# Kernel optimization log

Hardware: AMD Instinct MI355X
Metric: run time of the kernel (lower is better)

The kernel has to match this reference:

```python
import jax, jax.numpy as jnp
import numpy as np

SPARQ = 32
NEG = -32000.0


def sparq_masked_bmm(a, b, xs, xs_mask, value):
    # a: [N,A,B], b: [N,C,B], xs/xs_mask: [N,A,Z]
    N, A, B = a.shape
    C = b.shape[1]
    xs = jnp.clip(xs, 0, C - 1)
    _, a_idx = jax.lax.top_k(jnp.abs(a), SPARQ)              # SparQ: keep top-32 |q| dims
    a_mask = jnp.zeros_like(a).at[
        jnp.arange(N)[:, None, None], jnp.arange(A)[None, :, None], a_idx].set(1.0)
    ts = jnp.einsum('nab,ncb->nac', a * a_mask, b)           # [N,A,C]
    ys = jnp.take_along_axis(ts, xs, axis=-1)                # [N,A,Z]
    return jnp.where(xs_mask > 0.5, ys, value)


def forward_mask(w0, k_budget, q, k):
    # q: [NH, A, HID], k: [NH, T_SRC, HID]; returns additive mask [NH, A, T_SRC]
    NH, A, HID = q.shape
    T_SRC = k.shape[1]
    start = T_SRC - A + 1
    tsrcs_f = jnp.arange(start, start + A).astype(jnp.float32)   # [A]
    ws = jnp.full((A,), float(w0), jnp.float32)
    Zc = 2 * k_budget + 8                                        # static cap on unique pixel count
    z = jnp.arange(Zc)
    pixels = jnp.broadcast_to(jnp.where(z < k_budget, z, 0)[None, None, :], (NH, A, Zc)).astype(jnp.int32)
    pmask = jnp.broadcast_to((z < w0).astype(jnp.float32)[None, None, :], (NH, A, Zc))
    need = (ws < tsrcs_f)[None, :, None]                         # computed ONCE, as in torch
    w = w0
    while True:  # static python loop: w doubles until T_SRC
        txs = jnp.round(pixels * (tsrcs_f / ws)[None, :, None]).astype(jnp.int32)
        scores = sparq_masked_bmm(q, k, txs, pmask, NEG)
        tks = jnp.clip(jnp.round(ws / tsrcs_f * k_budget), 1.0,
                       jnp.minimum(ws - 1.0, float(Zc - 1))).astype(jnp.int32)[None, :, None]
        _, idx = jax.lax.top_k(scores, Zc)
        new_pixels = jnp.take_along_axis(pixels, idx, axis=-1)
        new_mask = (z[None, None, :] < tks).astype(jnp.float32)
        pixels = jnp.where(need, new_pixels, pixels)
        pmask = jnp.where(need, new_mask, pmask)
        # tree doubling: each pixel splits into up to 2 children at the new scale
        ws_new = jnp.minimum(tsrcs_f, ws * 2.0)
        scale = (ws_new / ws)[None, :, None]
        ps_start = jnp.round(pixels * scale).astype(jnp.int32)
        ps_end = jnp.round((pixels + 1) * scale).astype(jnp.int32)
        counts = ps_end - ps_start
        reps = jnp.arange(2, dtype=jnp.float32)[None, None, None, :] * pmask[..., None]
        reps = jnp.minimum(reps, jnp.maximum(counts - 1, 0)[..., None].astype(jnp.float32)).astype(jnp.int32)
        ps = (ps_start[..., None] + reps).reshape(NH * A, Zc * 2)
        # emulate sort + unique_consecutive + compacting scatter (duplicates -> -1 tail)
        ps = jnp.sort(ps, axis=-1)
        is_new = jnp.concatenate([jnp.ones((NH * A, 1), bool), ps[:, 1:] != ps[:, :-1]], axis=1)
        rank = jnp.cumsum(is_new, axis=-1) - 1
        res = jnp.full_like(ps, -1).at[jnp.arange(NH * A)[:, None], rank].set(ps)
        res = res.reshape(NH, A, 2 * Zc)[:, :, :Zc]              # static truncation (valid count <= 2k+1)
        pmask = (res >= 0).astype(jnp.float32)
        pixels = jnp.where(res >= 0, res, 0)
        ws = ws_new
        if w == T_SRC:
            break
        w = min(T_SRC, w * 2)
    pixels = (pixels.astype(jnp.float32) * pmask).astype(jnp.int32)
    ret = jnp.full((NH, A, T_SRC), NEG, jnp.float32)
    ret = ret.at[jnp.arange(NH)[:, None, None], jnp.arange(A)[None, :, None], pixels].set(0.0)
    return ret


def tree_attention(q, k, v, mask, k_budget, w0):
    N, H, T_SRC, HID = k.shape
    T_DST = q.shape[2]
    t_dense = max(0, k_budget - T_SRC + T_DST)
    outs = []
    if t_dense > 0:
        s = jnp.einsum('nhqd,nhkd->nhqk', q[:, :, :t_dense], k) + mask[:, :, :t_dense]
        outs.append(jnp.einsum('nhqk,nhkd->nhqd', jax.nn.softmax(s, axis=-1), v))
    if T_DST - t_dense > 0:
        qs = q[:, :, t_dense:]
        ms = forward_mask(w0, k_budget,
                          qs.reshape(N * H, -1, HID),
                          k.reshape(N * H, T_SRC, HID)).reshape(N, H, -1, T_SRC)
        s = jnp.einsum('nhqd,nhkd->nhqk', qs, k) + mask[:, :, t_dense:] + ms
        outs.append(jnp.einsum('nhqk,nhkd->nhqd', jax.nn.softmax(s, axis=-1), v))
    return jnp.concatenate(outs, axis=2)


def setup_inputs():
    key = jax.random.key(0)
    kq, kk, kv = jax.random.split(key, 3)
    N, H, T, HID = 1, 8, 2048, 64
    q = jax.random.normal(kq, (N, H, T, HID), jnp.float32)
    k = jax.random.normal(kk, (N, H, T, HID), jnp.float32)
    v = jax.random.normal(kv, (N, H, T, HID), jnp.float32)
    causal = jnp.tril(jnp.ones((T, T), bool))
    mask = jnp.where(causal, 0.0, NEG)[None, None].astype(jnp.float32)
    return {"q": q, "k": k, "v": v, "mask": mask}


def reference(q, k, v, mask):
    return tree_attention(q, k, v, mask, 512, 64)
```

## Files before the change

kernel.cpp:

```cpp
#include <hip/hip_runtime.h>
#include <math.h>

constexpr int HID    = 64;
constexpr int TT     = 2048;
constexpr int NHEAD  = 8;
constexpr int TDENSE = 512;
constexpr int ZC     = 1032;
constexpr int BITW   = 1024;

__device__ __forceinline__ float waveSum(float v) {
#pragma unroll
    for (int o = 32; o > 0; o >>= 1) v += __shfl_xor(v, o, 64);
    return v;
}
__device__ __forceinline__ int waveSumI(int v) {
#pragma unroll
    for (int o = 32; o > 0; o >>= 1) v += __shfl_xor(v, o, 64);
    return v;
}
__device__ __forceinline__ float waveMax(float v) {
#pragma unroll
    for (int o = 32; o > 0; o >>= 1) v = fmaxf(v, __shfl_xor(v, o, 64));
    return v;
}
__device__ __forceinline__ unsigned orderKey(float f) {
    unsigned u = __float_as_uint(f);
    return (u & 0x80000000u) ? ~u : (u | 0x80000000u);
}
__device__ __forceinline__ float dot4(float4 a, float4 b) {
    return fmaf(a.x, b.x, fmaf(a.y, b.y, fmaf(a.z, b.z, a.w * b.w)));
}
__device__ __forceinline__ float dotRow64(const float4* __restrict__ kr,
                                          const float4* __restrict__ qs) {
    float s0 = 0.f, s1 = 0.f, s2 = 0.f, s3 = 0.f;
#pragma unroll 2
    for (int i = 0; i < 4; i++) {
        float4 ka = kr[4*i+0], kb = kr[4*i+1], kc = kr[4*i+2], kd = kr[4*i+3];
        float4 qa = qs[4*i+0], qb = qs[4*i+1], qc = qs[4*i+2], qd = qs[4*i+3];
        s0 += dot4(ka, qa); s1 += dot4(kb, qb);
        s2 += dot4(kc, qc); s3 += dot4(kd, qd);
    }
    return (s0 + s1) + (s2 + s3);
}

struct __align__(16) SMem {
    float qf[HID];
    float aq[HID];
    float qm[HID];
    float partial[256];
    unsigned short pixA[ZC];
    unsigned short pixB[ZC];
    unsigned skey[ZC];
    unsigned bitmap[BITW];
    unsigned hist[4][256];
    float red[8];
    int scal[8];
    unsigned wsum[4];
};

__global__ __launch_bounds__(256)
void tree_attn_kernel(const float* __restrict__ q, const float* __restrict__ k,
                      const float* __restrict__ v, float* __restrict__ out) {
    __shared__ SMem sm;
    const int t    = 2047 - (int)blockIdx.x;
    const int h    = blockIdx.y;
    const int tid  = threadIdx.x;
    const int lane = tid & 63;
    const int wave = tid >> 6;
    const int sub  = lane & 15;
    const int grp  = lane >> 4;

    const float* qrow = q + (size_t)(h * TT + t) * HID;
    const float* kh   = k + (size_t)h * TT * HID;
    const float* vh   = v + (size_t)h * TT * HID;
    float*       orow = out + (size_t)(h * TT + t) * HID;

    if (tid < HID) sm.qf[tid] = qrow[tid];
    __syncthreads();

    if (t < TDENSE) {
        const int nk = t + 1;
        float* f = (float*)sm.skey;
        {
            int z = tid;
            for (; z + 256 < nk; z += 512) {
                float s0 = dotRow64((const float4*)(kh + (size_t)z * HID), (const float4*)sm.qf);
                float s1 = dotRow64((const float4*)(kh + (size_t)(z + 256) * HID), (const float4*)sm.qf);
                f[z] = s0; f[z + 256] = s1;
            }
            if (z < nk)
                f[z] = dotRow64((const float4*)(kh + (size_t)z * HID), (const float4*)sm.qf);
        }
        __syncthreads();
        float m = -3.0e38f;
        for (int z = tid; z < nk; z += 256) m = fmaxf(m, f[z]);
        m = waveMax(m);
        if (lane == 0) sm.red[wave] = m;
        __syncthreads();
        m = fmaxf(fmaxf(sm.red[0], sm.red[1]), fmaxf(sm.red[2], sm.red[3]));
        __syncthreads();
        float ls = 0.f;
        for (int z = tid; z < nk; z += 256) { float e = expf(f[z] - m); f[z] = e; ls += e; }
        ls = waveSum(ls);
        if (lane == 0) sm.red[4 + wave] = ls;
        __syncthreads();
        ls = sm.red[4] + sm.red[5] + sm.red[6] + sm.red[7];
        float4 acc = {0.f, 0.f, 0.f, 0.f};
        for (int z = (wave << 2) + grp; z < nk; z += 16) {
            float w = f[z];
            const float4 vv = *reinterpret_cast<const float4*>(vh + (size_t)z * HID + (sub << 2));
            acc.x = fmaf(w, vv.x, acc.x); acc.y = fmaf(w, vv.y, acc.y);
            acc.z = fmaf(w, vv.z, acc.z); acc.w = fmaf(w, vv.w, acc.w);
        }
#pragma unroll
        for (int o = 16; o <= 32; o <<= 1) {
            acc.x += __shfl_xor(acc.x, o, 64); acc.y += __shfl_xor(acc.y, o, 64);
            acc.z += __shfl_xor(acc.z, o, 64); acc.w += __shfl_xor(acc.w, o, 64);
        }
        if (grp == 0) reinterpret_cast<float4*>(sm.partial)[wave * 16 + sub] = acc;
        __syncthreads();
        if (tid < HID) {
            float o = sm.partial[tid] + sm.partial[64 + tid] + sm.partial[128 + tid] + sm.partial[192 + tid];
            orow[tid] = o / ls;
        }
        return;
    }

    const int a     = t - TDENSE;
    const int tsrci = TDENSE + 1 + a;
    const float tsrc = (float)tsrci;

    if (tid < HID) sm.aq[tid] = fabsf(sm.qf[tid]);
    __syncthreads();
    if (tid < HID) {
        float me = sm.aq[tid]; int c = 0;
#pragma unroll
        for (int i = 0; i < HID; i++) {
            float o = sm.aq[i];
            c += (o > me) || (o == me && i < tid);
        }
        sm.qm[tid] = (c < 32) ? sm.qf[tid] : 0.0f;
    }
    for (int z = tid; z < ZC; z += 256) sm.pixA[z] = (z < 512) ? (unsigned short)z : (unsigned short)0;
    for (int z = tid; z < 1024; z += 256) ((unsigned*)sm.hist)[z] = 0;
    __syncthreads();

    unsigned short* cur = sm.pixA;
    unsigned short* nxt = sm.pixB;
    int U = 64;
    float ws = 64.0f;
    int pmaxb = 511;

    for (int it = 0; it < 6; it++) {
        if (ws == tsrc) break;
        const float wsn   = fminf(tsrc, ws * 2.0f);
        const float ratio = tsrc / ws;

        {
            int z = tid;
            for (; z + 256 < U; z += 512) {
                int pA = cur[z], pB = cur[z + 256];
                int txA = min(max((int)rintf((float)pA * ratio), 0), TT - 1);
                int txB = min(max((int)rintf((float)pB * ratio), 0), TT - 1);
                float sA = dotRow64((const float4*)(kh + (size_t)txA * HID), (const float4*)sm.qm);
                float sB = dotRow64((const float4*)(kh + (size_t)txB * HID), (const float4*)sm.qm);
                unsigned kA = orderKey(sA), kB = orderKey(sB);
                sm.skey[z] = kA; sm.skey[z + 256] = kB;
                atomicAdd(&sm.hist[wave][kA >> 24], 1u);
                atomicAdd(&sm.hist[wave][kB >> 24], 1u);
            }
            if (z < U) {
                int p  = cur[z];
                int tx = min(max((int)rintf((float)p * ratio), 0), TT - 1);
                float s = dotRow64((const float4*)(kh + (size_t)tx * HID), (const float4*)sm.qm);
                unsigned kk2 = orderKey(s);
                sm.skey[z] = kk2;
                atomicAdd(&sm.hist[wave][kk2 >> 24], 1u);
            }
        }
        float tkf = rintf((ws / tsrc) * 512.0f);
        tkf = fminf(fmaxf(tkf, 1.0f), fminf(ws - 1.0f, 1031.0f));
        const int tks = (int)tkf;
        __syncthreads();

        unsigned thr = 0u;
        if (tks < U) {
            int bs = 24;
            for (;;) {
                if (wave == 0) {
                    const int i0 = 4 * lane;
                    int c0 = 0, c1 = 0, c2 = 0, c3 = 0;
#pragma unroll
                    for (int w = 0; w < 4; w++) {
                        c0 += (int)sm.hist[w][i0 + 0]; c1 += (int)sm.hist[w][i0 + 1];
                        c2 += (int)sm.hist[w][i0 + 2]; c3 += (int)sm.hist[w][i0 + 3];
                    }
#pragma unroll
                    for (int w = 0; w < 4; w++) {
                        sm.hist[w][i0 + 0] = 0; sm.hist[w][i0 + 1] = 0;
                        sm.hist[w][i0 + 2] = 0; sm.hist[w][i0 + 3] = 0;
                    }
                    const unsigned pref = (bs == 24) ? 0u : (unsigned)sm.scal[1];
                    const int wnt = (bs == 24) ? tks : sm.scal[0];
                    int x = c0 + c1 + c2 + c3;
#pragma unroll
                    for (int o = 1; o < 64; o <<= 1) {
                        int y = __shfl_up(x, o, 64);
                        if (lane >= o) x += y;
                    }
                    const int T = __shfl(x, 63, 64);
                    const int R = T - wnt;
                    int p3 = x, p2 = p3 - c3, p1 = p2 - c2, p0 = p1 - c1, pm1 = p0 - c0;
                    int b = -1, nw = 0, cc = 0;
                    if      (p0 > R && pm1 <= R) { b = i0 + 0; nw = p0 - R; cc = c0; }
                    else if (p1 > R && p0  <= R) { b = i0 + 1; nw = p1 - R; cc = c1; }
                    else if (p2 > R && p1  <= R) { b = i0 + 2; nw = p2 - R; cc = c2; }
                    else if (p3 > R && p2  <= R) { b = i0 + 3; nw = p3 - R; cc = c3; }
                    if (b >= 0) {
                        sm.scal[0] = nw;
                        sm.scal[1] = (int)(pref | ((unsigned)b << bs));
                        sm.scal[2] = cc;
                        sm.scal[3] = (cc == nw || bs == 0) ? 1 : 0;
                    }
                }
                __syncthreads();
                if (sm.scal[3]) { thr = (unsigned)sm.scal[1]; break; }
                const unsigned pref = (unsigned)sm.scal[1];
                bs -= 8;
                for (int z = tid; z < U; z += 256) {
                    unsigned key = sm.skey[z];
                    if ((key >> (bs + 8)) == (pref >> (bs + 8)))
                        atomicAdd(&sm.hist[wave][(key >> bs) & 255u], 1u);
                }
                __syncthreads();
            }
        } else {
            for (int z = tid; z < 1024; z += 256) ((unsigned*)sm.hist)[z] = 0;
        }

        const float scale = wsn / ws;
        const int pmax_new = min(32767, (int)rintf((float)(pmaxb + 1) * scale));
        const int nwords = (pmax_new >> 5) + 1;
        for (int w0 = tid; w0 < nwords; w0 += 256) sm.bitmap[w0] = 0;
        __syncthreads();
        for (int z = tid; z < ZC; z += 256) {
            int p = cur[z];
            float pf = (float)p;
            int ps0 = (int)rintf(pf * scale);
            ps0 = min(ps0, 32767);
            atomicOr(&sm.bitmap[ps0 >> 5], 1u << (ps0 & 31));
            if (z < U && sm.skey[z] >= thr) {
                int ps1 = (int)rintf((pf + 1.0f) * scale);
                if (ps1 - ps0 >= 2) {
                    int ch = min(ps0 + 1, 32767);
                    atomicOr(&sm.bitmap[ch >> 5], 1u << (ch & 31));
                }
            }
        }
        __syncthreads();

        const int base = tid * 4;
        unsigned b0 = (base + 0 < nwords) ? sm.bitmap[base + 0] : 0u;
        unsigned b1 = (base + 1 < nwords) ? sm.bitmap[base + 1] : 0u;
        unsigned b2 = (base + 2 < nwords) ? sm.bitmap[base + 2] : 0u;
        unsigned b3 = (base + 3 < nwords) ? sm.bitmap[base + 3] : 0u;
        int myc = __popc(b0) + __popc(b1) + __popc(b2) + __popc(b3);
        int x = myc;
#pragma unroll
        for (int o = 1; o < 64; o <<= 1) {
            int y = __shfl_up(x, o, 64);
            if (lane >= o) x += y;
        }
        if (lane == 63) sm.wsum[wave] = (unsigned)x;
        __syncthreads();
        int wOff = 0;
        for (int wv = 0; wv < wave; wv++) wOff += (int)sm.wsum[wv];
        const int total = (int)(sm.wsum[0] + sm.wsum[1] + sm.wsum[2] + sm.wsum[3]);
        const int newU = min(total, ZC);
        int pos = wOff + x - myc;
#pragma unroll
        for (int w0 = 0; w0 < 4; w0++) {
            unsigned bits = (w0 == 0) ? b0 : (w0 == 1) ? b1 : (w0 == 2) ? b2 : b3;
            int vbase = (base + w0) << 5;
            while (bits) {
                int b = __ffs(bits) - 1;
                bits &= bits - 1;
                if (pos < ZC) nxt[pos] = (unsigned short)(vbase + b);
                pos++;
            }
        }
        for (int z = newU + tid; z < ZC; z += 256) nxt[z] = 0;
        __syncthreads();

        unsigned short* tmp = cur; cur = nxt; nxt = tmp;
        U = newU;
        ws = wsn;
        pmaxb = pmax_new;
    }

    int ca = 0;
    for (int z = tid; z < U; z += 256) ca += (cur[z] < tsrci) ? 1 : 0;
    ca = waveSumI(ca);
    if (lane == 0) sm.scal[4 + wave] = ca;
    __syncthreads();
    const int Uatt = sm.scal[4] + sm.scal[5] + sm.scal[6] + sm.scal[7];
    __syncthreads();

    float* f = (float*)sm.skey;
    {
        int z = tid;
        for (; z + 256 < Uatt; z += 512) {
            float s0 = dotRow64((const float4*)(kh + (size_t)cur[z] * HID), (const float4*)sm.qf);
            float s1 = dotRow64((const float4*)(kh + (size_t)cur[z + 256] * HID), (const float4*)sm.qf);
            f[z] = s0; f[z + 256] = s1;
        }
        if (z < Uatt)
            f[z] = dotRow64((const float4*)(kh + (size_t)cur[z] * HID), (const float4*)sm.qf);
    }
    __syncthreads();
    float m = -3.0e38f;
    for (int z = tid; z < Uatt; z += 256) m = fmaxf(m, f[z]);
    m = waveMax(m);
    if (lane == 0) sm.red[wave] = m;
    __syncthreads();
    m = fmaxf(fmaxf(sm.red[0], sm.red[1]), fmaxf(sm.red[2], sm.red[3]));
    __syncthreads();
    float ls = 0.f;
    for (int z = tid; z < Uatt; z += 256) { float e = expf(f[z] - m); f[z] = e; ls += e; }
    ls = waveSum(ls);
    if (lane == 0) sm.red[4 + wave] = ls;
    __syncthreads();
    ls = sm.red[4] + sm.red[5] + sm.red[6] + sm.red[7];
    float4 acc = {0.f, 0.f, 0.f, 0.f};
    for (int z = (wave << 2) + grp; z < Uatt; z += 16) {
        float w = f[z];
        const float4 vv = *reinterpret_cast<const float4*>(vh + (size_t)cur[z] * HID + (sub << 2));
        acc.x = fmaf(w, vv.x, acc.x); acc.y = fmaf(w, vv.y, acc.y);
        acc.z = fmaf(w, vv.z, acc.z); acc.w = fmaf(w, vv.w, acc.w);
    }
#pragma unroll
    for (int o = 16; o <= 32; o <<= 1) {
        acc.x += __shfl_xor(acc.x, o, 64); acc.y += __shfl_xor(acc.y, o, 64);
        acc.z += __shfl_xor(acc.z, o, 64); acc.w += __shfl_xor(acc.w, o, 64);
    }
    if (grp == 0) reinterpret_cast<float4*>(sm.partial)[wave * 16 + sub] = acc;
    __syncthreads();
    if (tid < HID) {
        float o = sm.partial[tid] + sm.partial[64 + tid] + sm.partial[128 + tid] + sm.partial[192 + tid];
        orow[tid] = o / ls;
    }
}

extern "C" void kernel_launch(void* const* d_in, const int* in_sizes, int n_in,
                              void* d_out, int out_size, void* d_ws, size_t ws_size,
                              hipStream_t stream) {
    (void)in_sizes; (void)n_in; (void)d_ws; (void)ws_size; (void)out_size;
    const float* q = (const float*)d_in[0];
    const float* k = (const float*)d_in[1];
    const float* v = (const float*)d_in[2];
    float* out = (float*)d_out;
    dim3 grid(TT, NHEAD);
    tree_attn_kernel<<<grid, 256, 0, stream>>>(q, k, v, out);
}
```

Baseline: 1.211 ms.

## Merge bitmap atomics across wave lanes and shrink LDS histogram and bitmap

Result: slower. 1.447 ms (+19.6%).

```diff
diff --git a/kernel.cpp b/kernel.cpp
--- a/kernel.cpp
+++ b/kernel.cpp
@@ -6,7 +6,7 @@
 constexpr int NHEAD  = 8;
 constexpr int TDENSE = 512;
 constexpr int ZC     = 1032;
-constexpr int BITW   = 1024;
+constexpr int BITW   = 520;
 
 __device__ __forceinline__ float waveSum(float v) {
 #pragma unroll
@@ -43,6 +43,19 @@
     return (s0 + s1) + (s2 + s3);
 }
 
+__device__ __forceinline__ void mergedAtomicOr(unsigned* bm, unsigned word, unsigned bits,
+                                               bool valid, int lane) {
+    unsigned w = valid ? word : 0xFFFFFFFFu;
+#pragma unroll
+    for (int off = 1; off < 64; off <<= 1) {
+        unsigned ow = __shfl_down(w, off, 64);
+        unsigned ob = __shfl_down(bits, off, 64);
+        if (ow == w) bits |= ob;
+    }
+    unsigned pw = __shfl_up(w, 1, 64);
+    if (valid && (lane == 0 || pw != w)) atomicOr(&bm[w], bits);
+}
+
 struct __align__(16) SMem {
     float qf[HID];
     float aq[HID];
@@ -52,7 +65,7 @@
     unsigned short pixB[ZC];
     unsigned skey[ZC];
     unsigned bitmap[BITW];
-    unsigned hist[4][256];
+    unsigned hist[256];
     float red[8];
     int scal[8];
     unsigned wsum[4];
@@ -142,7 +155,7 @@
         sm.qm[tid] = (c < 32) ? sm.qf[tid] : 0.0f;
     }
     for (int z = tid; z < ZC; z += 256) sm.pixA[z] = (z < 512) ? (unsigned short)z : (unsigned short)0;
-    for (int z = tid; z < 1024; z += 256) ((unsigned*)sm.hist)[z] = 0;
+    sm.hist[tid] = 0;
     __syncthreads();
 
     unsigned short* cur = sm.pixA;
@@ -166,8 +179,8 @@
                 float sB = dotRow64((const float4*)(kh + (size_t)txB * HID), (const float4*)sm.qm);
                 unsigned kA = orderKey(sA), kB = orderKey(sB);
                 sm.skey[z] = kA; sm.skey[z + 256] = kB;
-                atomicAdd(&sm.hist[wave][kA >> 24], 1u);
-                atomicAdd(&sm.hist[wave][kB >> 24], 1u);
+                atomicAdd(&sm.hist[kA >> 24], 1u);
+                atomicAdd(&sm.hist[kB >> 24], 1u);
             }
             if (z < U) {
                 int p  = cur[z];
@@ -175,7 +188,7 @@
                 float s = dotRow64((const float4*)(kh + (size_t)tx * HID), (const float4*)sm.qm);
                 unsigned kk2 = orderKey(s);
                 sm.skey[z] = kk2;
-                atomicAdd(&sm.hist[wave][kk2 >> 24], 1u);
+                atomicAdd(&sm.hist[kk2 >> 24], 1u);
             }
         }
         float tkf = rintf((ws / tsrc) * 512.0f);
@@ -189,17 +202,10 @@
             for (;;) {
                 if (wave == 0) {
                     const int i0 = 4 * lane;
-                    int c0 = 0, c1 = 0, c2 = 0, c3 = 0;
-#pragma unroll
-                    for (int w = 0; w < 4; w++) {
-                        c0 += (int)sm.hist[w][i0 + 0]; c1 += (int)sm.hist[w][i0 + 1];
-                        c2 += (int)sm.hist[w][i0 + 2]; c3 += (int)sm.hist[w][i0 + 3];
-                    }
-#pragma unroll
-                    for (int w = 0; w < 4; w++) {
-                        sm.hist[w][i0 + 0] = 0; sm.hist[w][i0 + 1] = 0;
-                        sm.hist[w][i0 + 2] = 0; sm.hist[w][i0 + 3] = 0;
-                    }
+                    int c0 = (int)sm.hist[i0 + 0], c1 = (int)sm.hist[i0 + 1];
+                    int c2 = (int)sm.hist[i0 + 2], c3 = (int)sm.hist[i0 + 3];
+                    sm.hist[i0 + 0] = 0; sm.hist[i0 + 1] = 0;
+                    sm.hist[i0 + 2] = 0; sm.hist[i0 + 3] = 0;
                     const unsigned pref = (bs == 24) ? 0u : (unsigned)sm.scal[1];
                     const int wnt = (bs == 24) ? tks : sm.scal[0];
                     int x = c0 + c1 + c2 + c3;
@@ -230,32 +236,36 @@
                 for (int z = tid; z < U; z += 256) {
                     unsigned key = sm.skey[z];
                     if ((key >> (bs + 8)) == (pref >> (bs + 8)))
-                        atomicAdd(&sm.hist[wave][(key >> bs) & 255u], 1u);
+                        atomicAdd(&sm.hist[(key >> bs) & 255u], 1u);
                 }
                 __syncthreads();
             }
         } else {
-            for (int z = tid; z < 1024; z += 256) ((unsigned*)sm.hist)[z] = 0;
+            sm.hist[tid] = 0;
         }
 
         const float scale = wsn / ws;
-        const int pmax_new = min(32767, (int)rintf((float)(pmaxb + 1) * scale));
+        const int pmax_new = min(BITW * 32 - 1, (int)rintf((float)(pmaxb + 1) * scale));
         const int nwords = (pmax_new >> 5) + 1;
         for (int w0 = tid; w0 < nwords; w0 += 256) sm.bitmap[w0] = 0;
         __syncthreads();
-        for (int z = tid; z < ZC; z += 256) {
-            int p = cur[z];
+        for (int z = tid; z < 1280; z += 256) {
+            bool valid = z < ZC;
+            int p = valid ? cur[z] : 0;
+            int ps0 = min((int)rintf((float)p * scale), BITW * 32 - 1);
+            mergedAtomicOr(sm.bitmap, (unsigned)(ps0 >> 5), 1u << (ps0 & 31), valid, lane);
+        }
+        const int Upad = (U + 255) & ~255;
+        for (int z = tid; z < Upad; z += 256) {
+            bool valid = z < U;
+            int p = valid ? cur[z] : 0;
+            bool sel = valid && (sm.skey[z] >= thr);
             float pf = (float)p;
             int ps0 = (int)rintf(pf * scale);
-            ps0 = min(ps0, 32767);
-            atomicOr(&sm.bitmap[ps0 >> 5], 1u << (ps0 & 31));
-            if (z < U && sm.skey[z] >= thr) {
-                int ps1 = (int)rintf((pf + 1.0f) * scale);
-                if (ps1 - ps0 >= 2) {
-                    int ch = min(ps0 + 1, 32767);
-                    atomicOr(&sm.bitmap[ch >> 5], 1u << (ch & 31));
-                }
-            }
+            int ps1 = (int)rintf((pf + 1.0f) * scale);
+            bool emit = sel && (ps1 - ps0 >= 2);
+            int ch = min(ps0 + 1, BITW * 32 - 1);
+            mergedAtomicOr(sm.bitmap, (unsigned)(ch >> 5), 1u << (ch & 31), emit, lane);
         }
         __syncthreads();
 
```
